# Optimization experiments

Hardware: AMD Instinct MI355X
Metric: run time of the kernel (lower is better)

The kernel has to match this reference:

```python
import jax, jax.numpy as jnp
import numpy as np

NUM_EXPERTS = 32
TOP_K = 4
HIDDEN = 2048
INTER = 768


def setup_inputs() -> dict:
    key = jax.random.key(0)
    k1, k2, k3, k4 = jax.random.split(key, 4)
    hidden_states = jax.random.normal(k1, (4, 512, HIDDEN), dtype=jnp.float32)
    gate = jax.random.normal(k2, (HIDDEN, NUM_EXPERTS), dtype=jnp.float32) * 0.02
    gate_up_proj = jax.random.normal(k3, (NUM_EXPERTS, HIDDEN, 2 * INTER), dtype=jnp.float32) * 0.02
    down_proj = jax.random.normal(k4, (NUM_EXPERTS, INTER, HIDDEN), dtype=jnp.float32) * 0.02
    return {"hidden_states": hidden_states, "gate": gate,
            "gate_up_proj": gate_up_proj, "down_proj": down_proj}


def reference(hidden_states, gate, gate_up_proj, down_proj):
    batch_size = hidden_states.shape[0]
    x = hidden_states.reshape(-1, HIDDEN)  # (T, D)
    num_tokens = x.shape[0]

    # Router
    router_logits = jnp.einsum('TD,DE->TE', x, gate)
    routing_weights = jax.nn.softmax(router_logits.astype(jnp.float32), axis=-1)
    top_k_weights, top_k_indices = jax.lax.top_k(routing_weights, TOP_K)
    top_k_weights = top_k_weights / top_k_weights.sum(axis=-1, keepdims=True)
    top_k_weights = top_k_weights.astype(x.dtype)

    # Scatter top-k weights into full (T, E) matrix
    router_weights = jnp.zeros((num_tokens, NUM_EXPERTS), dtype=x.dtype)
    token_indices = jnp.broadcast_to(jnp.arange(num_tokens)[:, None], top_k_indices.shape)
    router_weights = router_weights.at[token_indices, top_k_indices].set(top_k_weights)

    # Dense all-expert experts pass (faithful to original: computes every expert per token)
    gate_up = jnp.einsum('TD,EDF->TEF', x, gate_up_proj)  # (T, E, 2F)
    g, u = jnp.split(gate_up, 2, axis=-1)
    gated = u * jax.nn.silu(g)  # (T, E, F)
    next_states = jnp.einsum('TEF,EFD->TED', gated, down_proj)
    next_states = (next_states * router_weights[..., None]).sum(axis=1)  # (T, D)
    return next_states.reshape(batch_size, -1, HIDDEN)
```

## Files before the change

kernel.cpp:

```cpp
#include <hip/hip_runtime.h>

#define T_TOKENS 2048
#define HIDDEN   2048
#define NEXPERT  32
#define TOPK     4
#define INTER    768
#define GUF      (2*INTER)
#define NPAIRS   (T_TOKENS*TOPK)
#define BM       256
#define BK       32
#define MT_MAX   63
#define NT1      6
#define NT2      8
#define NK1      (HIDDEN/BK)
#define NK2      (INTER/BK)

typedef short  bh8 __attribute__((ext_vector_type(8)));
typedef float  fx4 __attribute__((ext_vector_type(4)));

#define AS1 __attribute__((address_space(1)))
#define AS3 __attribute__((address_space(3)))

__device__ __forceinline__ void gload_lds16(const void* g, const void* lds_generic){
    __builtin_amdgcn_global_load_lds(
        (const AS1 void*)(unsigned long long)g,
        (AS3 void*)(unsigned int)(unsigned long long)lds_generic,
        16, 0, 0);
}

__device__ __forceinline__ unsigned int pack2bf(float a, float b){
    unsigned ua = __float_as_uint(a) + 0x8000u;
    unsigned ub = __float_as_uint(b) + 0x8000u;
    return __builtin_amdgcn_perm(ub, ua, 0x07060302u);
}
__device__ __forceinline__ unsigned short f2bfu(float f){
    return (unsigned short)((__float_as_uint(f) + 0x8000u) >> 16);
}
__device__ __forceinline__ float bf2f(unsigned short s){
    return __uint_as_float(((unsigned)s)<<16);
}

__global__ void cvt_x_k(const float* __restrict__ x, unsigned short* __restrict__ xb){
    int i = (blockIdx.x*256 + threadIdx.x)*8;
    float4 a = *(const float4*)(x+i);
    float4 b = *(const float4*)(x+i+4);
    uint4 o;
    o.x = pack2bf(a.x,a.y); o.y = pack2bf(a.z,a.w);
    o.z = pack2bf(b.x,b.y); o.w = pack2bf(b.z,b.w);
    *(uint4*)(xb+i) = o;
}

__global__ void router_k(const float* __restrict__ x, const float* __restrict__ gate,
                         int* __restrict__ topk_id, float* __restrict__ topk_w,
                         int* __restrict__ counts){
    const int t = blockIdx.x;
    const int l = threadIdx.x;
    const float* xr = x + (size_t)t*HIDDEN;
    float acc[NEXPERT];
#pragma unroll
    for (int e=0;e<NEXPERT;e++) acc[e]=0.f;
    for (int d=l; d<HIDDEN; d+=64){
        float xv = xr[d];
        const float4* g4 = (const float4*)(gate + (size_t)d*NEXPERT);
#pragma unroll
        for (int i=0;i<8;i++){
            float4 g = g4[i];
            acc[i*4+0] += xv*g.x; acc[i*4+1] += xv*g.y;
            acc[i*4+2] += xv*g.z; acc[i*4+3] += xv*g.w;
        }
    }
#pragma unroll
    for (int e=0;e<NEXPERT;e++){
#pragma unroll
        for (int m=1;m<64;m<<=1) acc[e] += __shfl_xor(acc[e], m, 64);
    }
    int ids[TOPK]; float lv[TOPK];
#pragma unroll
    for (int k=0;k<TOPK;k++){
        float m=-1e30f; int mi=0;
#pragma unroll
        for (int e=0;e<NEXPERT;e++){ if (acc[e]>m){ m=acc[e]; mi=e; } }
        ids[k]=mi; lv[k]=m; acc[mi]=-1e30f;
    }
    float ex[TOPK]; float s=0.f;
#pragma unroll
    for (int k=0;k<TOPK;k++){ ex[k]=__expf(lv[k]-lv[0]); s+=ex[k]; }
    if (l==0){
        float inv = 1.f/s;
#pragma unroll
        for (int k=0;k<TOPK;k++){
            topk_id[t*TOPK+k]=ids[k];
            topk_w[t*TOPK+k]=ex[k]*inv;
            atomicAdd(&counts[ids[k]],1);
        }
    }
}

__global__ void sched_k(const int* __restrict__ counts, int* __restrict__ offs,
                        int* __restrict__ cursors, int* __restrict__ nmt,
                        int* __restrict__ te, int* __restrict__ tr0, int* __restrict__ trn){
    if (threadIdx.x==0 && blockIdx.x==0){
        int tot=0, nm=0;
        for (int e=0;e<NEXPERT;e++){
            int c = counts[e];
            offs[e]=tot; cursors[e]=tot;
            for (int s=0;s<c;s+=BM){
                te[nm]=e; tr0[nm]=tot+s; trn[nm]=(c-s)<BM?(c-s):BM; nm++;
            }
            tot+=c;
        }
        *nmt = nm;
    }
}

__global__ void scatter_k(const int* __restrict__ topk_id, const float* __restrict__ topk_w,
                          int* __restrict__ cursors, int* __restrict__ pair_tok,
                          float* __restrict__ pair_w){
    int g = blockIdx.x*256 + threadIdx.x;
    int e = topk_id[g];
    float w = topk_w[g];
    int pos = atomicAdd(&cursors[e],1);
    pair_tok[pos] = g>>2;
    pair_w[pos]  = w;
}

#define TILE_DECODE(NTC)                                           \
    const int nwg = gridDim.x;                                     \
    const int q = nwg>>3, r = nwg&7;                               \
    const int xcd = blockIdx.x & 7, bidx = blockIdx.x >> 3;        \
    const int L = (xcd<r ? xcd*(q+1) : r*(q+1)+(xcd-r)*q) + bidx;  \
    const int mt = L / (NTC), nt = L % (NTC);                      \
    if (mt >= *nmt) return;                                        \
    const int e = te[mt], row0 = tr0[mt], rows = trn[mt];

#define MFMA16(A,B,C) __builtin_amdgcn_mfma_f32_16x16x32_bf16(A,B,C,0,0,0)

#define COMPUTE(BUF) do{                                                        \
    const unsigned short* _Ak = As[BUF];                                        \
    const char* _Bb = (const char*)Bs[BUF];                                     \
    bh8 _a0 = *(const bh8*)(_Ak + (wr*64      + l15)*32 + ((kb^sA)<<3));        \
    bh8 _a1 = *(const bh8*)(_Ak + (wr*64 + 16 + l15)*32 + ((kb^sA)<<3));        \
    bh8 _a2 = *(const bh8*)(_Ak + (wr*64 + 32 + l15)*32 + ((kb^sA)<<3));        \
    bh8 _a3 = *(const bh8*)(_Ak + (wr*64 + 48 + l15)*32 + ((kb^sA)<<3));        \
    _Pragma("unroll")                                                           \
    for (int c=0;c<4;c++){                                                      \
        const int bc = wc*64 + c*16 + l15;                                      \
        bh8 _b = *(const bh8*)(_Bb + bc*80 + ((kb ^ ((bc>>3)&3))<<4));          \
        acc[0][c] = MFMA16(_a0,_b,acc[0][c]);                                   \
        acc[1][c] = MFMA16(_a1,_b,acc[1][c]);                                   \
        acc[2][c] = MFMA16(_a2,_b,acc[2][c]);                                   \
        acc[3][c] = MFMA16(_a3,_b,acc[3][c]);                                   \
    } }while(0)

#define WRITEB(BUF) do{ char* _bb = (char*)Bs[BUF];                             \
    *(unsigned*)(_bb + wb      ) = pack2bf(rv0.x, rv1.x);                       \
    *(unsigned*)(_bb + wb +  80) = pack2bf(rv0.y, rv1.y);                       \
    *(unsigned*)(_bb + wb + 160) = pack2bf(rv0.z, rv1.z);                       \
    *(unsigned*)(_bb + wb + 240) = pack2bf(rv0.w, rv1.w); }while(0)

__global__ __launch_bounds__(1024,4) void gemm1_k(
        const unsigned short* __restrict__ xb, const float* __restrict__ gup,
        const int* __restrict__ nmt, const int* __restrict__ te,
        const int* __restrict__ tr0, const int* __restrict__ trn,
        const int* __restrict__ pair_tok,
        unsigned short* __restrict__ gu){
    __shared__ __align__(16) unsigned short As[2][BM*32];
    __shared__ __align__(16) unsigned short Bs[2][256*40];
    __shared__ int s_tok[BM];

    TILE_DECODE(NT1)
    const int n0 = nt*256;

    const int t = threadIdx.x;
    if (t < BM){
        int p = row0 + t; if (p > NPAIRS-1) p = NPAIRS-1;
        s_tok[t] = pair_tok[p];
    }
    __syncthreads();

    const int w = t>>6, lane = t&63;
    const int l15 = lane & 15, kb = lane >> 4;
    const int wr = w & 3, wc = w >> 2;
    const int sA = (l15>>1)&3;

    const int arow = w*16 + (lane>>2);
    const int ck0 = (lane&3) ^ ((lane>>3)&3);
    const unsigned short* asrc = xb + (size_t)s_tok[arow]*HIDDEN + ck0*8;

    const int tlow = t & 63, th = t >> 6;
    const int col4 = tlow*4, bd0 = th*2;
    const int gq = (tlow>>1)&3;
    const unsigned wb = (unsigned)(col4*80 + (((bd0>>3) ^ gq)<<4) + (bd0&7)*2);
    const float* bsrc = gup + (size_t)e*HIDDEN*GUF + (size_t)bd0*GUF + (n0 + col4);

    fx4 acc[4][4];
#pragma unroll
    for (int i=0;i<4;i++)
#pragma unroll
        for (int j=0;j<4;j++) acc[i][j] = (fx4)0.f;

    float4 rv0, rv1;
#define LOADB1(KS) do{ const float* _bp = bsrc + (size_t)(KS)*BK*GUF;           \
    rv0 = *(const float4*)(_bp); rv1 = *(const float4*)(_bp + GUF); }while(0)
#define STAGEA1(KS,BUF) gload_lds16(asrc + (KS)*BK, &As[BUF][(w*16)*32])

    STAGEA1(0,0); LOADB1(0);
    __syncthreads();
    WRITEB(0);
    __syncthreads();

    for (int k=0;k<NK1;k++){
        const int kn = k+1;
        if (kn < NK1){ LOADB1(kn); STAGEA1(kn, kn&1); }
        COMPUTE(k&1);
        __syncthreads();
        if (kn < NK1) WRITEB(kn&1);
        __syncthreads();
    }

#pragma unroll
    for (int mr=0;mr<4;mr++){
#pragma unroll
        for (int qq=0;qq<4;qq++){
            int row = wr*64 + mr*16 + kb*4 + qq;
            if (row < rows){
                size_t prow = (size_t)(row0 + row)*GUF + n0 + wc*64 + l15;
#pragma unroll
                for (int c=0;c<4;c++)
                    gu[prow + c*16] = f2bfu(acc[mr][c][qq]);
            }
        }
    }
#undef LOADB1
#undef STAGEA1
}

__global__ void silu_k(const unsigned short* __restrict__ gu,
                       const float* __restrict__ pair_w,
                       unsigned short* __restrict__ gated){
    const int t = threadIdx.x;
    const int r = (t >= 96) ? 1 : 0;
    const int jg = t - r*96;
    const int p = blockIdx.x*2 + r;
    bh8 g8 = *(const bh8*)(gu + (size_t)p*GUF + jg*8);
    bh8 u8 = *(const bh8*)(gu + (size_t)p*GUF + INTER + jg*8);
    float wgt = pair_w[p];
    bh8 o;
#pragma unroll
    for (int j=0;j<8;j++){
        float g = bf2f((unsigned short)g8[j]);
        float u = bf2f((unsigned short)u8[j]);
        float sil = g / (1.f + __expf(-g));
        o[j] = (short)f2bfu(sil*u*wgt);
    }
    *(bh8*)(gated + (size_t)p*INTER + jg*8) = o;
}

__global__ __launch_bounds__(1024,4) void gemm2_k(
        const unsigned short* __restrict__ gated, const float* __restrict__ down,
        const int* __restrict__ nmt, const int* __restrict__ te,
        const int* __restrict__ tr0, const int* __restrict__ trn,
        const int* __restrict__ pair_tok, float* __restrict__ out){
    __shared__ __align__(16) unsigned short As[2][BM*32];
    __shared__ __align__(16) unsigned short Bs[2][256*40];
    __shared__ int s_tok[BM];

    TILE_DECODE(NT2)
    const int n0 = nt*256;

    const int t = threadIdx.x;
    if (t < BM){
        int p = row0 + t; if (p > NPAIRS-1) p = NPAIRS-1;
        s_tok[t] = pair_tok[p];
    }
    __syncthreads();

    const int w = t>>6, lane = t&63;
    const int l15 = lane & 15, kb = lane >> 4;
    const int wr = w & 3, wc = w >> 2;
    const int sA = (l15>>1)&3;

    const int arow = w*16 + (lane>>2);
    const int ck0 = (lane&3) ^ ((lane>>3)&3);
    int ap = row0 + arow; if (ap > NPAIRS-1) ap = NPAIRS-1;
    const unsigned short* asrc = gated + (size_t)ap*INTER + ck0*8;

    const int tlow = t & 63, th = t >> 6;
    const int col4 = tlow*4, bd0 = th*2;
    const int gq = (tlow>>1)&3;
    const unsigned wb = (unsigned)(col4*80 + (((bd0>>3) ^ gq)<<4) + (bd0&7)*2);
    const float* bsrc = down + (size_t)e*INTER*HIDDEN + (size_t)bd0*HIDDEN + (n0 + col4);

    fx4 acc[4][4];
#pragma unroll
    for (int i=0;i<4;i++)
#pragma unroll
        for (int j=0;j<4;j++) acc[i][j] = (fx4)0.f;

    float4 rv0, rv1;
#define LOADB2(KS) do{ const float* _bp = bsrc + (size_t)(KS)*BK*HIDDEN;        \
    rv0 = *(const float4*)(_bp); rv1 = *(const float4*)(_bp + HIDDEN); }while(0)
#define STAGEA2(KS,BUF) gload_lds16(asrc + (KS)*BK, &As[BUF][(w*16)*32])

    STAGEA2(0,0); LOADB2(0);
    __syncthreads();
    WRITEB(0);
    __syncthreads();

    for (int k=0;k<NK2;k++){
        const int kn = k+1;
        if (kn < NK2){ LOADB2(kn); STAGEA2(kn, kn&1); }
        COMPUTE(k&1);
        __syncthreads();
        if (kn < NK2) WRITEB(kn&1);
        __syncthreads();
    }

#pragma unroll
    for (int mr=0;mr<4;mr++){
#pragma unroll
        for (int qq=0;qq<4;qq++){
            int row = wr*64 + mr*16 + kb*4 + qq;
            if (row < rows){
                float* orow = out + (size_t)s_tok[row]*HIDDEN + n0 + wc*64 + l15;
#pragma unroll
                for (int c=0;c<4;c++)
                    atomicAdd(orow + c*16, acc[mr][c][qq]);
            }
        }
    }
#undef LOADB2
#undef STAGEA2
}

extern "C" void kernel_launch(void* const* d_in, const int* in_sizes, int n_in,
                              void* d_out, int out_size, void* d_ws, size_t ws_size,
                              hipStream_t stream){
    const float* x    = (const float*)d_in[0];
    const float* gate = (const float*)d_in[1];
    const float* gup  = (const float*)d_in[2];
    const float* down = (const float*)d_in[3];
    float* out = (float*)d_out;
    char*  ws  = (char*)d_ws;

    int*   topk_id  = (int*)  (ws + 0x00000);
    float* topk_w   = (float*)(ws + 0x08000);
    int*   counts   = (int*)  (ws + 0x10000);
    int*   cursors  = (int*)  (ws + 0x10080);
    int*   offs     = (int*)  (ws + 0x10100);
    int*   nmt      = (int*)  (ws + 0x10180);
    int*   te       = (int*)  (ws + 0x10200);
    int*   tr0      = (int*)  (ws + 0x10400);
    int*   trn      = (int*)  (ws + 0x10600);
    int*   pair_tok = (int*)  (ws + 0x10800);
    float* pair_w   = (float*)(ws + 0x18800);
    unsigned short* gated = (unsigned short*)(ws + 0x21000);
    unsigned short* xb    = (unsigned short*)(ws + 0xC60000);
    unsigned short* gu    = (unsigned short*)(ws + 0x1460000);

    hipMemsetAsync(d_out, 0, (size_t)out_size*sizeof(float), stream);
    hipMemsetAsync(counts, 0, NEXPERT*sizeof(int), stream);

    cvt_x_k  <<<T_TOKENS*HIDDEN/(256*8), 256, 0, stream>>>(x, xb);
    router_k <<<T_TOKENS, 64, 0, stream>>>(x, gate, topk_id, topk_w, counts);
    sched_k  <<<1, 64, 0, stream>>>(counts, offs, cursors, nmt, te, tr0, trn);
    scatter_k<<<NPAIRS/256, 256, 0, stream>>>(topk_id, topk_w, cursors, pair_tok, pair_w);
    gemm1_k  <<<MT_MAX*NT1, 1024, 0, stream>>>(xb, gup, nmt, te, tr0, trn, pair_tok, gu);
    silu_k   <<<NPAIRS/2, 192, 0, stream>>>(gu, pair_w, gated);
    gemm2_k  <<<MT_MAX*NT2, 1024, 0, stream>>>(gated, down, nmt, te, tr0, trn, pair_tok, out);
}
```

Before: 490.2 us.

## Pre-transpose weights to bf16 tiles, fuse SiLU into gemm1, shrink tiles

Two new kernels convert the expert weights to bf16 each call and store them pre-tiled in K-major 32-wide blocks. The GEMMs can then stage both operands into LDS with direct global-to-LDS DMA instead of register loads, conversion and packed LDS writes. Gemm1 interleaves gate and up columns so the SiLU, the multiply and the routing weight are applied in its epilogue, which removes the separate silu kernel and the gu intermediate. Tiles shrink to 128 rows with 256-thread blocks and tile order becomes m-fastest. In exchange, the full weight tensors are read and rewritten in bf16 on every call, which adds memory traffic for all experts.

```diff
diff --git a/kernel.cpp b/kernel.cpp
--- a/kernel.cpp
+++ b/kernel.cpp
@@ -5,13 +5,12 @@
 #define NEXPERT  32
 #define TOPK     4
 #define INTER    768
-#define GUF      (2*INTER)
 #define NPAIRS   (T_TOKENS*TOPK)
-#define BM       256
+#define BM       128
 #define BK       32
-#define MT_MAX   63
-#define NT1      6
-#define NT2      8
+#define MT_MAX   95
+#define NT1      12
+#define NT2      16
 #define NK1      (HIDDEN/BK)
 #define NK2      (INTER/BK)
 
@@ -35,9 +34,6 @@
 }
 __device__ __forceinline__ unsigned short f2bfu(float f){
     return (unsigned short)((__float_as_uint(f) + 0x8000u) >> 16);
-}
-__device__ __forceinline__ float bf2f(unsigned short s){
-    return __uint_as_float(((unsigned)s)<<16);
 }
 
 __global__ void cvt_x_k(const float* __restrict__ x, unsigned short* __restrict__ xb){
@@ -124,74 +120,109 @@
     pair_w[pos]  = w;
 }
 
-#define TILE_DECODE(NTC)                                           \
+__global__ __launch_bounds__(256) void wt1_k(const float* __restrict__ gup,
+                                             unsigned short* __restrict__ wT1){
+    __shared__ unsigned short L[128*40];
+    const int b = blockIdx.x;
+    const int ks = b & 63, nt = (b>>6) % NT1, e = b / (64*NT1);
+    const int t = threadIdx.x;
+    const int s = t>>7, t7 = t&127;
+    const int kk = t7>>2, fq = (t7&3)*16;
+    const float* src = gup + ((size_t)e*HIDDEN + (size_t)ks*BK + kk)*(2*INTER)
+                           + (s ? 768 + nt*64 : nt*64) + fq;
+    float4 v0 = ((const float4*)src)[0];
+    float4 v1 = ((const float4*)src)[1];
+    float4 v2 = ((const float4*)src)[2];
+    float4 v3 = ((const float4*)src)[3];
+    const int fb = s*64 + fq;
+    L[(fb+ 0)*40+kk]=f2bfu(v0.x); L[(fb+ 1)*40+kk]=f2bfu(v0.y);
+    L[(fb+ 2)*40+kk]=f2bfu(v0.z); L[(fb+ 3)*40+kk]=f2bfu(v0.w);
+    L[(fb+ 4)*40+kk]=f2bfu(v1.x); L[(fb+ 5)*40+kk]=f2bfu(v1.y);
+    L[(fb+ 6)*40+kk]=f2bfu(v1.z); L[(fb+ 7)*40+kk]=f2bfu(v1.w);
+    L[(fb+ 8)*40+kk]=f2bfu(v2.x); L[(fb+ 9)*40+kk]=f2bfu(v2.y);
+    L[(fb+10)*40+kk]=f2bfu(v2.z); L[(fb+11)*40+kk]=f2bfu(v2.w);
+    L[(fb+12)*40+kk]=f2bfu(v3.x); L[(fb+13)*40+kk]=f2bfu(v3.y);
+    L[(fb+14)*40+kk]=f2bfu(v3.z); L[(fb+15)*40+kk]=f2bfu(v3.w);
+    __syncthreads();
+    const int f2 = t>>1, kc = t&1;
+    uint4 o0 = *(const uint4*)&L[f2*40 + kc*16];
+    uint4 o1 = *(const uint4*)&L[f2*40 + kc*16 + 8];
+    unsigned short* dst = wT1 + (size_t)b*4096 + t*16;
+    ((uint4*)dst)[0] = o0;
+    ((uint4*)dst)[1] = o1;
+}
+
+__global__ __launch_bounds__(256) void wt2_k(const float* __restrict__ down,
+                                             unsigned short* __restrict__ wT2){
+    __shared__ unsigned short L[128*40];
+    const int b = blockIdx.x;
+    const int ks = b % NK2, nt = (b/NK2) % NT2, e = b / (NK2*NT2);
+    const int t = threadIdx.x;
+    const int kk = t>>3, nq = (t&7)*16;
+    const float* src = down + ((size_t)e*INTER + (size_t)ks*BK + kk)*HIDDEN
+                            + nt*128 + nq;
+    float4 v0 = ((const float4*)src)[0];
+    float4 v1 = ((const float4*)src)[1];
+    float4 v2 = ((const float4*)src)[2];
+    float4 v3 = ((const float4*)src)[3];
+    L[(nq+ 0)*40+kk]=f2bfu(v0.x); L[(nq+ 1)*40+kk]=f2bfu(v0.y);
+    L[(nq+ 2)*40+kk]=f2bfu(v0.z); L[(nq+ 3)*40+kk]=f2bfu(v0.w);
+    L[(nq+ 4)*40+kk]=f2bfu(v1.x); L[(nq+ 5)*40+kk]=f2bfu(v1.y);
+    L[(nq+ 6)*40+kk]=f2bfu(v1.z); L[(nq+ 7)*40+kk]=f2bfu(v1.w);
+    L[(nq+ 8)*40+kk]=f2bfu(v2.x); L[(nq+ 9)*40+kk]=f2bfu(v2.y);
+    L[(nq+10)*40+kk]=f2bfu(v2.z); L[(nq+11)*40+kk]=f2bfu(v2.w);
+    L[(nq+12)*40+kk]=f2bfu(v3.x); L[(nq+13)*40+kk]=f2bfu(v3.y);
+    L[(nq+14)*40+kk]=f2bfu(v3.z); L[(nq+15)*40+kk]=f2bfu(v3.w);
+    __syncthreads();
+    const int f2 = t>>1, kc = t&1;
+    uint4 o0 = *(const uint4*)&L[f2*40 + kc*16];
+    uint4 o1 = *(const uint4*)&L[f2*40 + kc*16 + 8];
+    unsigned short* dst = wT2 + (size_t)b*4096 + t*16;
+    ((uint4*)dst)[0] = o0;
+    ((uint4*)dst)[1] = o1;
+}
+
+#define TILE_DECODE()                                              \
     const int nwg = gridDim.x;                                     \
     const int q = nwg>>3, r = nwg&7;                               \
     const int xcd = blockIdx.x & 7, bidx = blockIdx.x >> 3;        \
     const int L = (xcd<r ? xcd*(q+1) : r*(q+1)+(xcd-r)*q) + bidx;  \
-    const int mt = L / (NTC), nt = L % (NTC);                      \
+    const int mt = L % MT_MAX, nt = L / MT_MAX;                    \
     if (mt >= *nmt) return;                                        \
     const int e = te[mt], row0 = tr0[mt], rows = trn[mt];
 
 #define MFMA16(A,B,C) __builtin_amdgcn_mfma_f32_16x16x32_bf16(A,B,C,0,0,0)
 
-#define COMPUTE(BUF) do{                                                        \
-    const unsigned short* _Ak = As[BUF];                                        \
-    const char* _Bb = (const char*)Bs[BUF];                                     \
-    bh8 _a0 = *(const bh8*)(_Ak + (wr*64      + l15)*32 + ((kb^sA)<<3));        \
-    bh8 _a1 = *(const bh8*)(_Ak + (wr*64 + 16 + l15)*32 + ((kb^sA)<<3));        \
-    bh8 _a2 = *(const bh8*)(_Ak + (wr*64 + 32 + l15)*32 + ((kb^sA)<<3));        \
-    bh8 _a3 = *(const bh8*)(_Ak + (wr*64 + 48 + l15)*32 + ((kb^sA)<<3));        \
-    _Pragma("unroll")                                                           \
-    for (int c=0;c<4;c++){                                                      \
-        const int bc = wc*64 + c*16 + l15;                                      \
-        bh8 _b = *(const bh8*)(_Bb + bc*80 + ((kb ^ ((bc>>3)&3))<<4));          \
-        acc[0][c] = MFMA16(_a0,_b,acc[0][c]);                                   \
-        acc[1][c] = MFMA16(_a1,_b,acc[1][c]);                                   \
-        acc[2][c] = MFMA16(_a2,_b,acc[2][c]);                                   \
-        acc[3][c] = MFMA16(_a3,_b,acc[3][c]);                                   \
-    } }while(0)
-
-#define WRITEB(BUF) do{ char* _bb = (char*)Bs[BUF];                             \
-    *(unsigned*)(_bb + wb      ) = pack2bf(rv0.x, rv1.x);                       \
-    *(unsigned*)(_bb + wb +  80) = pack2bf(rv0.y, rv1.y);                       \
-    *(unsigned*)(_bb + wb + 160) = pack2bf(rv0.z, rv1.z);                       \
-    *(unsigned*)(_bb + wb + 240) = pack2bf(rv0.w, rv1.w); }while(0)
-
-__global__ __launch_bounds__(1024,4) void gemm1_k(
-        const unsigned short* __restrict__ xb, const float* __restrict__ gup,
+__global__ __launch_bounds__(256,3) void gemm1_k(
+        const unsigned short* __restrict__ xb, const unsigned short* __restrict__ wT1,
         const int* __restrict__ nmt, const int* __restrict__ te,
         const int* __restrict__ tr0, const int* __restrict__ trn,
-        const int* __restrict__ pair_tok,
-        unsigned short* __restrict__ gu){
+        const int* __restrict__ pair_tok, const float* __restrict__ pair_w,
+        unsigned short* __restrict__ gated){
     __shared__ __align__(16) unsigned short As[2][BM*32];
-    __shared__ __align__(16) unsigned short Bs[2][256*40];
-    __shared__ int s_tok[BM];
-
-    TILE_DECODE(NT1)
-    const int n0 = nt*256;
+    __shared__ __align__(16) unsigned short Bs[2][BM*32];
+    __shared__ int   s_tok[BM];
+    __shared__ float s_w[BM];
+
+    TILE_DECODE()
+    const int n0 = nt*64;
 
     const int t = threadIdx.x;
     if (t < BM){
         int p = row0 + t; if (p > NPAIRS-1) p = NPAIRS-1;
         s_tok[t] = pair_tok[p];
+        s_w[t]   = pair_w[p];
     }
     __syncthreads();
 
     const int w = t>>6, lane = t&63;
     const int l15 = lane & 15, kb = lane >> 4;
-    const int wr = w & 3, wc = w >> 2;
-    const int sA = (l15>>1)&3;
-
-    const int arow = w*16 + (lane>>2);
-    const int ck0 = (lane&3) ^ ((lane>>3)&3);
-    const unsigned short* asrc = xb + (size_t)s_tok[arow]*HIDDEN + ck0*8;
-
-    const int tlow = t & 63, th = t >> 6;
-    const int col4 = tlow*4, bd0 = th*2;
-    const int gq = (tlow>>1)&3;
-    const unsigned wb = (unsigned)(col4*80 + (((bd0>>3) ^ gq)<<4) + (bd0&7)*2);
-    const float* bsrc = gup + (size_t)e*HIDDEN*GUF + (size_t)bd0*GUF + (n0 + col4);
+    const int wr = w & 1, wc = w >> 1;
+
+    const int ar0 = w*16 + (lane>>2), ar1 = 64 + ar0;
+    const unsigned short* asrc0 = xb + (size_t)s_tok[ar0]*HIDDEN + (lane&3)*8;
+    const unsigned short* asrc1 = xb + (size_t)s_tok[ar1]*HIDDEN + (lane&3)*8;
+    const unsigned short* bsrc = wT1 + ((size_t)(e*NT1 + nt)*NK1)*4096 + w*512 + lane*8;
 
     fx4 acc[4][4];
 #pragma unroll
@@ -199,74 +230,66 @@
 #pragma unroll
         for (int j=0;j<4;j++) acc[i][j] = (fx4)0.f;
 
-    float4 rv0, rv1;
-#define LOADB1(KS) do{ const float* _bp = bsrc + (size_t)(KS)*BK*GUF;           \
-    rv0 = *(const float4*)(_bp); rv1 = *(const float4*)(_bp + GUF); }while(0)
-#define STAGEA1(KS,BUF) gload_lds16(asrc + (KS)*BK, &As[BUF][(w*16)*32])
-
-    STAGEA1(0,0); LOADB1(0);
-    __syncthreads();
-    WRITEB(0);
-    __syncthreads();
-
+#define DMA1(BUF,KS) do{                                                        \
+    gload_lds16(asrc0 + (KS)*BK,            &As[BUF][ w*512      ]);            \
+    gload_lds16(asrc1 + (KS)*BK,            &As[BUF][2048 + w*512]);            \
+    gload_lds16(bsrc + (size_t)(KS)*4096,   &Bs[BUF][ w*512      ]);            \
+    gload_lds16(bsrc + (size_t)(KS)*4096+2048, &Bs[BUF][2048 + w*512]);         \
+}while(0)
+
+    DMA1(0,0);
     for (int k=0;k<NK1;k++){
-        const int kn = k+1;
-        if (kn < NK1){ LOADB1(kn); STAGEA1(kn, kn&1); }
-        COMPUTE(k&1);
         __syncthreads();
-        if (kn < NK1) WRITEB(kn&1);
-        __syncthreads();
-    }
-
-#pragma unroll
-    for (int mr=0;mr<4;mr++){
+        if (k+1 < NK1) DMA1((k+1)&1, k+1);
+        const unsigned short* Ak = As[k&1];
+        const unsigned short* Bk = Bs[k&1];
+        bh8 a0 = *(const bh8*)(Ak + (wr*64      + l15)*32 + kb*8);
+        bh8 a1 = *(const bh8*)(Ak + (wr*64 + 16 + l15)*32 + kb*8);
+        bh8 a2 = *(const bh8*)(Ak + (wr*64 + 32 + l15)*32 + kb*8);
+        bh8 a3 = *(const bh8*)(Ak + (wr*64 + 48 + l15)*32 + kb*8);
+#pragma unroll
+        for (int ni=0;ni<4;ni++){
+            const int br = (ni<2) ? (wc*32 + ni*16 + l15)
+                                  : (64 + wc*32 + (ni-2)*16 + l15);
+            bh8 b = *(const bh8*)(Bk + br*32 + kb*8);
+            acc[0][ni]=MFMA16(a0,b,acc[0][ni]);
+            acc[1][ni]=MFMA16(a1,b,acc[1][ni]);
+            acc[2][ni]=MFMA16(a2,b,acc[2][ni]);
+            acc[3][ni]=MFMA16(a3,b,acc[3][ni]);
+        }
+    }
+
+#pragma unroll
+    for (int mi=0;mi<4;mi++){
 #pragma unroll
         for (int qq=0;qq<4;qq++){
-            int row = wr*64 + mr*16 + kb*4 + qq;
+            int row = wr*64 + mi*16 + kb*4 + qq;
             if (row < rows){
-                size_t prow = (size_t)(row0 + row)*GUF + n0 + wc*64 + l15;
-#pragma unroll
-                for (int c=0;c<4;c++)
-                    gu[prow + c*16] = f2bfu(acc[mr][c][qq]);
+                float wgt = s_w[row];
+                size_t prow = (size_t)(row0 + row)*INTER + n0 + wc*32 + l15;
+#pragma unroll
+                for (int ni2=0;ni2<2;ni2++){
+                    float g = acc[mi][ni2][qq], u = acc[mi][ni2+2][qq];
+                    float sil = g / (1.f + __expf(-g));
+                    gated[prow + ni2*16] = f2bfu(sil*u*wgt);
+                }
             }
         }
     }
-#undef LOADB1
-#undef STAGEA1
-}
-
-__global__ void silu_k(const unsigned short* __restrict__ gu,
-                       const float* __restrict__ pair_w,
-                       unsigned short* __restrict__ gated){
-    const int t = threadIdx.x;
-    const int r = (t >= 96) ? 1 : 0;
-    const int jg = t - r*96;
-    const int p = blockIdx.x*2 + r;
-    bh8 g8 = *(const bh8*)(gu + (size_t)p*GUF + jg*8);
-    bh8 u8 = *(const bh8*)(gu + (size_t)p*GUF + INTER + jg*8);
-    float wgt = pair_w[p];
-    bh8 o;
-#pragma unroll
-    for (int j=0;j<8;j++){
-        float g = bf2f((unsigned short)g8[j]);
-        float u = bf2f((unsigned short)u8[j]);
-        float sil = g / (1.f + __expf(-g));
-        o[j] = (short)f2bfu(sil*u*wgt);
-    }
-    *(bh8*)(gated + (size_t)p*INTER + jg*8) = o;
-}
-
-__global__ __launch_bounds__(1024,4) void gemm2_k(
-        const unsigned short* __restrict__ gated, const float* __restrict__ down,
+#undef DMA1
+}
+
+__global__ __launch_bounds__(256,3) void gemm2_k(
+        const unsigned short* __restrict__ gated, const unsigned short* __restrict__ wT2,
         const int* __restrict__ nmt, const int* __restrict__ te,
         const int* __restrict__ tr0, const int* __restrict__ trn,
         const int* __restrict__ pair_tok, float* __restrict__ out){
     __shared__ __align__(16) unsigned short As[2][BM*32];
-    __shared__ __align__(16) unsigned short Bs[2][256*40];
+    __shared__ __align__(16) unsigned short Bs[2][BM*32];
     __shared__ int s_tok[BM];
 
-    TILE_DECODE(NT2)
-    const int n0 = nt*256;
+    TILE_DECODE()
+    const int n0 = nt*128;
 
     const int t = threadIdx.x;
     if (t < BM){
@@ -277,19 +300,14 @@
 
     const int w = t>>6, lane = t&63;
     const int l15 = lane & 15, kb = lane >> 4;
-    const int wr = w & 3, wc = w >> 2;
-    const int sA = (l15>>1)&3;
-
-    const int arow = w*16 + (lane>>2);
-    const int ck0 = (lane&3) ^ ((lane>>3)&3);
-    int ap = row0 + arow; if (ap > NPAIRS-1) ap = NPAIRS-1;
-    const unsigned short* asrc = gated + (size_t)ap*INTER + ck0*8;
-
-    const int tlow = t & 63, th = t >> 6;
-    const int col4 = tlow*4, bd0 = th*2;
-    const int gq = (tlow>>1)&3;
-    const unsigned wb = (unsigned)(col4*80 + (((bd0>>3) ^ gq)<<4) + (bd0&7)*2);
-    const float* bsrc = down + (size_t)e*INTER*HIDDEN + (size_t)bd0*HIDDEN + (n0 + col4);
+    const int wr = w & 1, wc = w >> 1;
+
+    const int ar0 = w*16 + (lane>>2), ar1 = 64 + ar0;
+    int ap0 = row0 + ar0; if (ap0 > NPAIRS-1) ap0 = NPAIRS-1;
+    int ap1 = row0 + ar1; if (ap1 > NPAIRS-1) ap1 = NPAIRS-1;
+    const unsigned short* asrc0 = gated + (size_t)ap0*INTER + (lane&3)*8;
+    const unsigned short* asrc1 = gated + (size_t)ap1*INTER + (lane&3)*8;
+    const unsigned short* bsrc = wT2 + ((size_t)(e*NT2 + nt)*NK2)*4096 + w*512 + lane*8;
 
     fx4 acc[4][4];
 #pragma unroll
@@ -297,40 +315,48 @@
 #pragma unroll
         for (int j=0;j<4;j++) acc[i][j] = (fx4)0.f;
 
-    float4 rv0, rv1;
-#define LOADB2(KS) do{ const float* _bp = bsrc + (size_t)(KS)*BK*HIDDEN;        \
-    rv0 = *(const float4*)(_bp); rv1 = *(const float4*)(_bp + HIDDEN); }while(0)
-#define STAGEA2(KS,BUF) gload_lds16(asrc + (KS)*BK, &As[BUF][(w*16)*32])
-
-    STAGEA2(0,0); LOADB2(0);
-    __syncthreads();
-    WRITEB(0);
-    __syncthreads();
-
+#define DMA2(BUF,KS) do{                                                        \
+    gload_lds16(asrc0 + (KS)*BK,            &As[BUF][ w*512      ]);            \
+    gload_lds16(asrc1 + (KS)*BK,            &As[BUF][2048 + w*512]);            \
+    gload_lds16(bsrc + (size_t)(KS)*4096,   &Bs[BUF][ w*512      ]);            \
+    gload_lds16(bsrc + (size_t)(KS)*4096+2048, &Bs[BUF][2048 + w*512]);         \
+}while(0)
+
+    DMA2(0,0);
     for (int k=0;k<NK2;k++){
-        const int kn = k+1;
-        if (kn < NK2){ LOADB2(kn); STAGEA2(kn, kn&1); }
-        COMPUTE(k&1);
         __syncthreads();
-        if (kn < NK2) WRITEB(kn&1);
-        __syncthreads();
-    }
-
-#pragma unroll
-    for (int mr=0;mr<4;mr++){
+        if (k+1 < NK2) DMA2((k+1)&1, k+1);
+        const unsigned short* Ak = As[k&1];
+        const unsigned short* Bk = Bs[k&1];
+        bh8 a0 = *(const bh8*)(Ak + (wr*64      + l15)*32 + kb*8);
+        bh8 a1 = *(const bh8*)(Ak + (wr*64 + 16 + l15)*32 + kb*8);
+        bh8 a2 = *(const bh8*)(Ak + (wr*64 + 32 + l15)*32 + kb*8);
+        bh8 a3 = *(const bh8*)(Ak + (wr*64 + 48 + l15)*32 + kb*8);
+#pragma unroll
+        for (int ni=0;ni<4;ni++){
+            const int br = wc*64 + ni*16 + l15;
+            bh8 b = *(const bh8*)(Bk + br*32 + kb*8);
+            acc[0][ni]=MFMA16(a0,b,acc[0][ni]);
+            acc[1][ni]=MFMA16(a1,b,acc[1][ni]);
+            acc[2][ni]=MFMA16(a2,b,acc[2][ni]);
+            acc[3][ni]=MFMA16(a3,b,acc[3][ni]);
+        }
+    }
+
+#pragma unroll
+    for (int mi=0;mi<4;mi++){
 #pragma unroll
         for (int qq=0;qq<4;qq++){
-            int row = wr*64 + mr*16 + kb*4 + qq;
+            int row = wr*64 + mi*16 + kb*4 + qq;
             if (row < rows){
                 float* orow = out + (size_t)s_tok[row]*HIDDEN + n0 + wc*64 + l15;
 #pragma unroll
-                for (int c=0;c<4;c++)
-                    atomicAdd(orow + c*16, acc[mr][c][qq]);
+                for (int ni=0;ni<4;ni++)
+                    atomicAdd(orow + ni*16, acc[mi][ni][qq]);
             }
         }
     }
-#undef LOADB2
-#undef STAGEA2
+#undef DMA2
 }
 
 extern "C" void kernel_launch(void* const* d_in, const int* in_sizes, int n_in,
@@ -356,7 +382,8 @@
     float* pair_w   = (float*)(ws + 0x18800);
     unsigned short* gated = (unsigned short*)(ws + 0x21000);
     unsigned short* xb    = (unsigned short*)(ws + 0xC60000);
-    unsigned short* gu    = (unsigned short*)(ws + 0x1460000);
+    unsigned short* wT1   = (unsigned short*)(ws + 0x1460000);
+    unsigned short* wT2   = (unsigned short*)(ws + 0xD460000);
 
     hipMemsetAsync(d_out, 0, (size_t)out_size*sizeof(float), stream);
     hipMemsetAsync(counts, 0, NEXPERT*sizeof(int), stream);
@@ -365,7 +392,10 @@
     router_k <<<T_TOKENS, 64, 0, stream>>>(x, gate, topk_id, topk_w, counts);
     sched_k  <<<1, 64, 0, stream>>>(counts, offs, cursors, nmt, te, tr0, trn);
     scatter_k<<<NPAIRS/256, 256, 0, stream>>>(topk_id, topk_w, cursors, pair_tok, pair_w);
-    gemm1_k  <<<MT_MAX*NT1, 1024, 0, stream>>>(xb, gup, nmt, te, tr0, trn, pair_tok, gu);
-    silu_k   <<<NPAIRS/2, 192, 0, stream>>>(gu, pair_w, gated);
-    gemm2_k  <<<MT_MAX*NT2, 1024, 0, stream>>>(gated, down, nmt, te, tr0, trn, pair_tok, out);
-}
+
+    wt1_k    <<<NEXPERT*NT1*NK1, 256, 0, stream>>>(gup,  wT1);
+    wt2_k    <<<NEXPERT*NT2*NK2, 256, 0, stream>>>(down, wT2);
+
+    gemm1_k  <<<MT_MAX*NT1, 256, 0, stream>>>(xb, wT1, nmt, te, tr0, trn, pair_tok, pair_w, gated);
+    gemm2_k  <<<MT_MAX*NT2, 256, 0, stream>>>(gated, wT2, nmt, te, tr0, trn, pair_tok, out);
+}
```

Result: slower. 505.8 us (+3.2%).
